# Optimization experiments

Hardware: AMD Instinct MI355X
Metric: run time of the kernel (lower is better)

The kernel has to match this reference:

```python
import jax, jax.numpy as jnp
import numpy as np

B, C, T = 64, 128, 500
N_RES, N_CLASSES = 2048, 10
DECAY_RES, DECAY_CLF = 0.9, 0.9
V_TH_RES, V_TH_CLF = 1.0, 1.0


def setup_inputs() -> dict:
    key = jax.random.key(0)
    k1, k2, k3, k4 = jax.random.split(key, 4)
    x = jax.random.normal(k1, (B, C, T), dtype=jnp.float32)
    # learned / fixed parameters sized per init_kwargs
    W_in = jax.random.normal(k2, (N_RES, C), dtype=jnp.float32) * (1.0 / np.sqrt(C))
    W_res = jax.random.normal(k3, (N_RES, N_RES), dtype=jnp.float32) * (1.0 / np.sqrt(N_RES))
    W_clf = jax.random.normal(k4, (N_CLASSES, N_RES), dtype=jnp.float32) * (1.0 / np.sqrt(N_RES))
    return {"x": x, "W_in": W_in, "W_res": W_res, "W_clf": W_clf}


def reference(x, W_in, W_res, W_clf):
    """x: (B, C, T). Returns (spike_counts (B, n_classes), reservoir_spikes_accum (B, n_reservoir)).
    LIF reservoir + single-voter LIF readout, no STDP updates (use_stdp=False path)."""
    Bb = x.shape[0]
    dtype = x.dtype

    def step(carry, x_t):  # x_t: (B, C)
        v_r, s_prev, v_c = carry
        # reservoir LIF: leak + feedforward input + recurrent spike input
        I = x_t @ W_in.T + s_prev @ W_res.T          # (B, N_RES)
        v_r = DECAY_RES * v_r + I
        s = (v_r >= V_TH_RES).astype(dtype)          # spike
        v_r = v_r * (1.0 - s)                        # reset fired neurons
        # classifier (STDPLayer forward, plasticity disabled)
        v_c = DECAY_CLF * v_c + s @ W_clf.T          # (B, N_CLASSES)
        c = (v_c >= V_TH_CLF).astype(dtype)
        v_c = v_c * (1.0 - c)
        return (v_r, s, v_c), (c, s)

    init = (jnp.zeros((Bb, N_RES), dtype),
            jnp.zeros((Bb, N_RES), dtype),
            jnp.zeros((Bb, N_CLASSES), dtype))
    xs = jnp.moveaxis(x, 2, 0)                       # (T, B, C)
    _, (clf_spikes, res_spikes) = jax.lax.scan(step, init, xs)
    spike_counts = clf_spikes.sum(axis=0)            # (B, N_CLASSES)
    reservoir_spikes_accum = res_spikes.sum(axis=0)  # (B, N_RES)
    return spike_counts, reservoir_spikes_accum
```

## Files before the change

kernel.cpp:

```cpp
#include <hip/hip_runtime.h>
#include <cstdint>
#include <cstddef>

#define B_    64
#define C_    128
#define T_    500
#define NRES  2048
#define NCLS  10

#define NWG   256
#define SL    8
#define NT    1024
#define WROW  520
#define WPIT  (4 * WROW)



#define WS_MASK0   0
#define WS_MASK1   16384
#define WS_CNT1    32768
#define WS_CNT2    34816
#define WS_FLAG    36864
#define WS_WORDS   13312
#define NGRP       8
#define GRPSZ      (NWG / NGRP)
#define NFLAG      16

typedef float v2f __attribute__((ext_vector_type(2)));

struct SMem {
  float    WtT2[SL][WPIT];
  float    WinT2[SL][C_];
  float    xs[B_][C_ + 1];
  unsigned mask[B_][65];
  float    g1buf[SL][B_];
  double   clfred[2][16][NCLS];
};

__global__ void zero_ws_kernel(unsigned* __restrict__ p, int n) {
  int i = blockIdx.x * blockDim.x + threadIdx.x;
  if (i < n) p[i] = 0u;
}

#define ACC2(ACC, WB, M0, M1, JB) do {                                        \
  const unsigned _lo = (unsigned)(((int)((M0) << (31 - (JB)))) >> 31) & (WB); \
  const unsigned _hi = (unsigned)(((int)((M1) << (31 - (JB)))) >> 31) & (WB); \
  v2f _m; _m.x = __uint_as_float(_lo); _m.y = __uint_as_float(_hi);           \
  (ACC) = (ACC) + _m;                                                         \
} while (0)

#define BT_STEP(X, D, MLO) do {                                            \
  const unsigned _y = (unsigned)__shfl_xor((int)(X), (D), 64);             \
  (X) = (b & (D)) ? (((X) & ~(MLO)) | ((_y >> (D)) & (MLO)))               \
                  : (((X) & (MLO)) | ((_y << (D)) & ~(MLO)));              \
} while (0)

#define BT_ALL(X) do {                 \
  BT_STEP(X, 16, 0x0000FFFFu);         \
  BT_STEP(X,  8, 0x00FF00FFu);         \
  BT_STEP(X,  4, 0x0F0F0F0Fu);         \
  BT_STEP(X,  2, 0x33333333u);         \
  BT_STEP(X,  1, 0x55555555u);         \
} while (0)

__global__ void __launch_bounds__(NT, 4)
reservoir_kernel(const float* __restrict__ x, const float* __restrict__ Win,
                 const float* __restrict__ Wres, const float* __restrict__ Wclf,
                 float* __restrict__ out, unsigned char* __restrict__ ws) {
  __shared__ SMem sm;
  const int w   = blockIdx.x;
  const int tid = threadIdx.x;
  const int b   = tid & 63;
  const int wid = tid >> 6;
  const int il  = wid & 7;
  const int h   = wid >> 3;
  const int blk = b & 3;
  const int g   = b >> 2;
  const int bat0 = h * 32 + g * 2;
  const int bat1 = bat0 + 1;
  const int iu  = __builtin_amdgcn_readfirstlane(w * SL + il);

  unsigned* gm0  = (unsigned*)(ws + WS_MASK0);
  unsigned* gm1  = (unsigned*)(ws + WS_MASK1);
  unsigned* cnt1 = (unsigned*)(ws + WS_CNT1 + (w & (NGRP - 1)) * 256);
  unsigned* cnt2 = (unsigned*)(ws + WS_CNT2);
  unsigned* flgb = (unsigned*)(ws + WS_FLAG);
  unsigned* myflag = flgb + (w & (NFLAG - 1)) * 256;

  {
    const int j0 = tid * 16;
    #pragma unroll
    for (int r4 = 0; r4 < 4; ++r4) {
      const int j   = j0 + r4 * 4;
      const int il2 = j >> 11;
      const int pos = j & 2047;
      const int bk  = pos >> 9;
      const int s   = pos & 511;
      const float4 v4 = *(const float4*)(Wres + (size_t)(w * SL + il2) * NRES + pos);
      *(float4*)(&sm.WtT2[il2][bk * WROW + s]) = v4;
    }
  }
  {
    const int il2 = tid >> 7, c = tid & 127;
    sm.WinT2[il2][c] = Win[(size_t)(w * SL + il2) * C_ + c];
  }

  float wcf[NCLS * 2];
  {
    const int j0 = tid * 2;
    #pragma unroll
    for (int c2 = 0; c2 < NCLS; ++c2)
      #pragma unroll
      for (int jj = 0; jj < 2; ++jj)
        wcf[c2 * 2 + jj] = Wclf[(size_t)c2 * NRES + j0 + jj];
  }

  float v = 0.f;
  int   cntr = 0;
  double vc = 0.0;
  int   cntc = 0;

  float xv[8];
  {
    const int p0 = tid * 8;
    #pragma unroll
    for (int r = 0; r < 8; ++r) xv[r] = x[(size_t)(p0 + r) * T_ + 0];
    #pragma unroll
    for (int r = 0; r < 8; ++r) {
      int p = p0 + r;
      sm.xs[p >> 7][p & 127] = xv[r];
    }
  }

  for (int t = 0; t < T_; ++t) {
    unsigned* gprev = (t & 1) ? gm0 : gm1;
    unsigned* gcur  = (t & 1) ? gm1 : gm0;

    {
      const int i32 = b & 31, hh = b >> 5;
      #pragma unroll
      for (int kk = 0; kk < 4; ++kk) {
        const int k = (wid << 2) | kk;
        unsigned xw = __hip_atomic_load(gprev + (k * 32 + i32) * 2 + hh,
                                        __ATOMIC_RELAXED, __HIP_MEMORY_SCOPE_AGENT);
        BT_ALL(xw);
        sm.mask[b][k] = xw;
      }
    }
    __syncthreads();

    if (t + 1 < T_) {
      const int p0 = tid * 8;
      #pragma unroll
      for (int r = 0; r < 8; ++r) xv[r] = x[(size_t)(p0 + r) * T_ + (t + 1)];
    }

    if (h == 0) {
      float g1 = 0.f;
      const float4* __restrict__ winp = (const float4*)&sm.WinT2[il][0];
      #pragma unroll 8
      for (int cq = 0; cq < 32; ++cq) {
        const float4 wv = winp[cq];
        const int c = cq * 4;
        g1 = fmaf(sm.xs[b][c + 0], wv.x, g1);
        g1 = fmaf(sm.xs[b][c + 1], wv.y, g1);
        g1 = fmaf(sm.xs[b][c + 2], wv.z, g1);
        g1 = fmaf(sm.xs[b][c + 3], wv.w, g1);
      }
      sm.g1buf[il][b] = g1;
    }

    v2f acc; acc.x = 0.f; acc.y = 0.f;
    {
      const float*    wbase = &sm.WtT2[il][blk * WROW];
      const unsigned* mr0   = &sm.mask[bat0][blk * 16];
      const unsigned* mr1   = &sm.mask[bat1][blk * 16];
      for (int wq = 0; wq < 16; ++wq) {
        const unsigned m0 = mr0[wq];
        const unsigned m1 = mr1[wq];
        const float4* q = (const float4*)(wbase + wq * 32);
        #pragma unroll
        for (int jq = 0; jq < 8; ++jq) {
          const float4 w4 = q[jq];
          const int jb = jq * 4;
          ACC2(acc, __float_as_uint(w4.x), m0, m1, jb + 0);
          ACC2(acc, __float_as_uint(w4.y), m0, m1, jb + 1);
          ACC2(acc, __float_as_uint(w4.z), m0, m1, jb + 2);
          ACC2(acc, __float_as_uint(w4.w), m0, m1, jb + 3);
        }
      }
    }
    const float aP = acc.x, aQ = acc.y;

    const float p1 = __shfl_xor(aP, 1), q1 = __shfl_xor(aQ, 1);
    const float p2 = __shfl_xor(aP, 2), q2 = __shfl_xor(aQ, 2);
    const float p3 = __shfl_xor(aP, 3), q3 = __shfl_xor(aQ, 3);
    const float g2u0 = __fadd_rn(__fadd_rn(__fadd_rn(aP, p1), p2), p3);
    const float g2u1 = __fadd_rn(__fadd_rn(__fadd_rn(aQ, q1), q2), q3);

    __syncthreads();

    {
      const int src = (b >> 1) * 4;
      const float r0 = __shfl(g2u0, src, 64);
      const float r1 = __shfl(g2u1, src, 64);
      const float g2m = (b & 1) ? r1 : r0;
      const float g1m = sm.g1buf[il][h * 32 + (b & 31)];
      const float I = __fadd_rn(g1m, g2m);
      v = __fadd_rn(__fmul_rn(0.9f, v), I);
      bool s = (b < 32) && (v >= 1.0f);
      if (s) { v = 0.f; cntr++; }
      unsigned long long bal = __ballot(s);
      if (b == 0)
        __hip_atomic_store(gcur + iu * 2 + h, (unsigned)bal,
                           __ATOMIC_RELAXED, __HIP_MEMORY_SCOPE_AGENT);
    }
    __syncthreads();

    if (tid == 0) {
      unsigned old = __hip_atomic_fetch_add(cnt1, 1u, __ATOMIC_RELEASE,
                                            __HIP_MEMORY_SCOPE_AGENT);
      if (old == (unsigned)(t + 1) * GRPSZ - 1u) {
        unsigned old2 = __hip_atomic_fetch_add(cnt2, 1u, __ATOMIC_ACQ_REL,
                                               __HIP_MEMORY_SCOPE_AGENT);
        if (old2 == (unsigned)(t + 1) * NGRP - 1u) {
          #pragma unroll
          for (int f = 0; f < NFLAG; ++f)
            __hip_atomic_store(flgb + f * 256, (unsigned)(t + 1),
                               __ATOMIC_RELEASE, __HIP_MEMORY_SCOPE_AGENT);
        }
      }
    }

    if (w < B_) {
      double pc[NCLS];
      #pragma unroll
      for (int c2 = 0; c2 < NCLS; ++c2) pc[c2] = 0.0;
      if (t > 0) {
        const int j0 = tid * 2;
        unsigned mw = sm.mask[w][j0 >> 5];
        #pragma unroll
        for (int jj = 0; jj < 2; ++jj) {
          if ((mw >> ((j0 + jj) & 31)) & 1u) {
            #pragma unroll
            for (int c2 = 0; c2 < NCLS; ++c2)
              pc[c2] += (double)wcf[c2 * 2 + jj];
          }
        }
      }
      #pragma unroll
      for (int off = 1; off < 64; off <<= 1) {
        #pragma unroll
        for (int c2 = 0; c2 < NCLS; ++c2)
          pc[c2] += __shfl_xor(pc[c2], off, 64);
      }
      if ((tid & 63) == 0) {
        #pragma unroll
        for (int c2 = 0; c2 < NCLS; ++c2) sm.clfred[t & 1][wid][c2] = pc[c2];
      }
    }

    if (w < B_ && tid < NCLS && t >= 2) {
      double sc = 0.0;
      #pragma unroll
      for (int q2 = 0; q2 < 16; ++q2) sc += sm.clfred[(t + 1) & 1][q2][tid];
      vc = 0.9 * vc + sc;
      if (vc >= 1.0) { vc = 0.0; cntc++; }
    }

    if (t + 1 < T_) {
      const int p0 = tid * 8;
      #pragma unroll
      for (int r = 0; r < 8; ++r) {
        int p = p0 + r;
        sm.xs[p >> 7][p & 127] = xv[r];
      }
    }

    if (tid == 0) {
      while (__hip_atomic_load(myflag, __ATOMIC_RELAXED,
                               __HIP_MEMORY_SCOPE_AGENT) < (unsigned)(t + 1))
        __builtin_amdgcn_s_sleep(1);
    }
    __syncthreads();
  }

  if (w < B_ && tid < NCLS) {
    double sc = 0.0;
    #pragma unroll
    for (int q2 = 0; q2 < 16; ++q2) sc += sm.clfred[1][q2][tid];
    vc = 0.9 * vc + sc;
    if (vc >= 1.0) { vc = 0.0; cntc++; }
  }
  {
    const int i32 = b & 31, hh = b >> 5;
    #pragma unroll
    for (int kk = 0; kk < 4; ++kk) {
      const int k = (wid << 2) | kk;
      unsigned xw = __hip_atomic_load(gm1 + (k * 32 + i32) * 2 + hh,
                                      __ATOMIC_RELAXED, __HIP_MEMORY_SCOPE_AGENT);
      BT_ALL(xw);
      sm.mask[b][k] = xw;
    }
  }
  __syncthreads();
  if (w < B_) {
    double pc[NCLS];
    #pragma unroll
    for (int c2 = 0; c2 < NCLS; ++c2) pc[c2] = 0.0;
    const int j0 = tid * 2;
    unsigned mw = sm.mask[w][j0 >> 5];
    #pragma unroll
    for (int jj = 0; jj < 2; ++jj) {
      if ((mw >> ((j0 + jj) & 31)) & 1u) {
        #pragma unroll
        for (int c2 = 0; c2 < NCLS; ++c2)
          pc[c2] += (double)wcf[c2 * 2 + jj];
      }
    }
    #pragma unroll
    for (int off = 1; off < 64; off <<= 1) {
      #pragma unroll
      for (int c2 = 0; c2 < NCLS; ++c2)
        pc[c2] += __shfl_xor(pc[c2], off, 64);
    }
    if ((tid & 63) == 0) {
      #pragma unroll
      for (int c2 = 0; c2 < NCLS; ++c2) sm.clfred[0][wid][c2] = pc[c2];
    }
  }
  __syncthreads();
  if (w < B_ && tid < NCLS) {
    double sc = 0.0;
    #pragma unroll
    for (int q2 = 0; q2 < 16; ++q2) sc += sm.clfred[0][q2][tid];
    vc = 0.9 * vc + sc;
    if (vc >= 1.0) cntc++;
    out[w * NCLS + tid] = (float)cntc;
  }
  if (b < 32)
    out[B_ * NCLS + (size_t)(h * 32 + b) * NRES + w * SL + il] = (float)cntr;
}

extern "C" void kernel_launch(void* const* d_in, const int* in_sizes, int n_in,
                              void* d_out, int out_size, void* d_ws, size_t ws_size,
                              hipStream_t stream) {
  const float* x    = (const float*)d_in[0];
  const float* Win  = (const float*)d_in[1];
  const float* Wres = (const float*)d_in[2];
  const float* Wclf = (const float*)d_in[3];
  float* out = (float*)d_out;
  unsigned char* ws = (unsigned char*)d_ws;

  hipLaunchKernelGGL(zero_ws_kernel, dim3((WS_WORDS + 255) / 256), dim3(256), 0, stream,
                     (unsigned*)ws, WS_WORDS);
  hipLaunchKernelGGL(reservoir_kernel, dim3(NWG), dim3(NT), 0, stream,
                     x, Win, Wres, Wclf, out, ws);
}
```

Baseline: 15.91 ms.

## Replace two-level atomic counter barrier with per-block arrival flags and checker block

Replaces the hierarchical fetch-add grid barrier with per-workgroup arrival slots that a single checker workgroup polls before publishing release flags. It also double-buffers the input slice in shared memory so one in-loop __syncthreads can be removed, computes the input projection in each wave rather than through a shared buffer, and restructures the classifier readout as one wave per class reading Wclf from global memory. The aim is to shorten the per-timestep critical path made of atomics and block barriers. The cost is a single polling workgroup that can become a serialization point, plus repeated global reads of Wclf.

```diff
diff --git a/kernel.cpp b/kernel.cpp
--- a/kernel.cpp
+++ b/kernel.cpp
@@ -18,23 +18,20 @@
 
 #define WS_MASK0   0
 #define WS_MASK1   16384
-#define WS_CNT1    32768
-#define WS_CNT2    34816
-#define WS_FLAG    36864
+#define WS_FLAG    32768
+#define WS_ARR     49152
 #define WS_WORDS   13312
-#define NGRP       8
-#define GRPSZ      (NWG / NGRP)
 #define NFLAG      16
+#define CHKWG      (NWG - 1)
 
 typedef float v2f __attribute__((ext_vector_type(2)));
 
 struct SMem {
   float    WtT2[SL][WPIT];
   float    WinT2[SL][C_];
-  float    xs[B_][C_ + 1];
+  float    xs2[2][B_][C_ + 1];
   unsigned mask[B_][65];
-  float    g1buf[SL][B_];
-  double   clfred[2][16][NCLS];
+  double   clfred2[2][NCLS];
 };
 
 __global__ void zero_ws_kernel(unsigned* __restrict__ p, int n) {
@@ -82,9 +79,8 @@
 
   unsigned* gm0  = (unsigned*)(ws + WS_MASK0);
   unsigned* gm1  = (unsigned*)(ws + WS_MASK1);
-  unsigned* cnt1 = (unsigned*)(ws + WS_CNT1 + (w & (NGRP - 1)) * 256);
-  unsigned* cnt2 = (unsigned*)(ws + WS_CNT2);
   unsigned* flgb = (unsigned*)(ws + WS_FLAG);
+  unsigned* arr  = (unsigned*)(ws + WS_ARR);
   unsigned* myflag = flgb + (w & (NFLAG - 1)) * 256;
 
   {
@@ -105,16 +101,6 @@
     sm.WinT2[il2][c] = Win[(size_t)(w * SL + il2) * C_ + c];
   }
 
-  float wcf[NCLS * 2];
-  {
-    const int j0 = tid * 2;
-    #pragma unroll
-    for (int c2 = 0; c2 < NCLS; ++c2)
-      #pragma unroll
-      for (int jj = 0; jj < 2; ++jj)
-        wcf[c2 * 2 + jj] = Wclf[(size_t)c2 * NRES + j0 + jj];
-  }
-
   float v = 0.f;
   int   cntr = 0;
   double vc = 0.0;
@@ -124,12 +110,13 @@
   {
     const int p0 = tid * 8;
     #pragma unroll
-    for (int r = 0; r < 8; ++r) xv[r] = x[(size_t)(p0 + r) * T_ + 0];
-    #pragma unroll
     for (int r = 0; r < 8; ++r) {
+      float z = x[(size_t)(p0 + r) * T_ + 0];
       int p = p0 + r;
-      sm.xs[p >> 7][p & 127] = xv[r];
-    }
+      sm.xs2[0][p >> 7][p & 127] = z;
+    }
+    #pragma unroll
+    for (int r = 0; r < 8; ++r) xv[r] = x[(size_t)(p0 + r) * T_ + 1];
   }
 
   for (int t = 0; t < T_; ++t) {
@@ -152,22 +139,30 @@
     if (t + 1 < T_) {
       const int p0 = tid * 8;
       #pragma unroll
-      for (int r = 0; r < 8; ++r) xv[r] = x[(size_t)(p0 + r) * T_ + (t + 1)];
-    }
-
-    if (h == 0) {
-      float g1 = 0.f;
+      for (int r = 0; r < 8; ++r) {
+        int p = p0 + r;
+        sm.xs2[(t + 1) & 1][p >> 7][p & 127] = xv[r];
+      }
+      if (t + 2 < T_) {
+        #pragma unroll
+        for (int r = 0; r < 8; ++r) xv[r] = x[(size_t)(p0 + r) * T_ + (t + 2)];
+      }
+    }
+
+    float g1 = 0.f;
+    if (b < 32) {
+      const int bat = h * 32 + b;
       const float4* __restrict__ winp = (const float4*)&sm.WinT2[il][0];
+      const float* __restrict__ xrow = &sm.xs2[t & 1][bat][0];
       #pragma unroll 8
       for (int cq = 0; cq < 32; ++cq) {
         const float4 wv = winp[cq];
         const int c = cq * 4;
-        g1 = fmaf(sm.xs[b][c + 0], wv.x, g1);
-        g1 = fmaf(sm.xs[b][c + 1], wv.y, g1);
-        g1 = fmaf(sm.xs[b][c + 2], wv.z, g1);
-        g1 = fmaf(sm.xs[b][c + 3], wv.w, g1);
-      }
-      sm.g1buf[il][b] = g1;
+        g1 = fmaf(xrow[c + 0], wv.x, g1);
+        g1 = fmaf(xrow[c + 1], wv.y, g1);
+        g1 = fmaf(xrow[c + 2], wv.z, g1);
+        g1 = fmaf(xrow[c + 3], wv.w, g1);
+      }
     }
 
     v2f acc; acc.x = 0.f; acc.y = 0.f;
@@ -198,15 +193,12 @@
     const float g2u0 = __fadd_rn(__fadd_rn(__fadd_rn(aP, p1), p2), p3);
     const float g2u1 = __fadd_rn(__fadd_rn(__fadd_rn(aQ, q1), q2), q3);
 
-    __syncthreads();
-
     {
       const int src = (b >> 1) * 4;
       const float r0 = __shfl(g2u0, src, 64);
       const float r1 = __shfl(g2u1, src, 64);
       const float g2m = (b & 1) ? r1 : r0;
-      const float g1m = sm.g1buf[il][h * 32 + (b & 31)];
-      const float I = __fadd_rn(g1m, g2m);
+      const float I = __fadd_rn(g1, g2m);
       v = __fadd_rn(__fmul_rn(0.9f, v), I);
       bool s = (b < 32) && (v >= 1.0f);
       if (s) { v = 0.f; cntr++; }
@@ -217,64 +209,52 @@
     }
     __syncthreads();
 
-    if (tid == 0) {
-      unsigned old = __hip_atomic_fetch_add(cnt1, 1u, __ATOMIC_RELEASE,
-                                            __HIP_MEMORY_SCOPE_AGENT);
-      if (old == (unsigned)(t + 1) * GRPSZ - 1u) {
-        unsigned old2 = __hip_atomic_fetch_add(cnt2, 1u, __ATOMIC_ACQ_REL,
-                                               __HIP_MEMORY_SCOPE_AGENT);
-        if (old2 == (unsigned)(t + 1) * NGRP - 1u) {
-          #pragma unroll
-          for (int f = 0; f < NFLAG; ++f)
-            __hip_atomic_store(flgb + f * 256, (unsigned)(t + 1),
-                               __ATOMIC_RELEASE, __HIP_MEMORY_SCOPE_AGENT);
+    if (tid == 0)
+      __hip_atomic_store(arr + w * 4, (unsigned)(t + 1),
+                         __ATOMIC_RELEASE, __HIP_MEMORY_SCOPE_AGENT);
+
+    if (w == CHKWG && wid == 0) {
+      const unsigned tgt = (unsigned)(t + 1);
+      for (;;) {
+        unsigned a0 = __hip_atomic_load(arr + (b +   0) * 4, __ATOMIC_RELAXED,
+                                        __HIP_MEMORY_SCOPE_AGENT);
+        unsigned a1 = __hip_atomic_load(arr + (b +  64) * 4, __ATOMIC_RELAXED,
+                                        __HIP_MEMORY_SCOPE_AGENT);
+        unsigned a2 = __hip_atomic_load(arr + (b + 128) * 4, __ATOMIC_RELAXED,
+                                        __HIP_MEMORY_SCOPE_AGENT);
+        unsigned a3 = __hip_atomic_load(arr + (b + 192) * 4, __ATOMIC_RELAXED,
+                                        __HIP_MEMORY_SCOPE_AGENT);
+        bool ok = (a0 >= tgt) & (a1 >= tgt) & (a2 >= tgt) & (a3 >= tgt);
+        if (__all(ok)) break;
+        __builtin_amdgcn_s_sleep(1);
+      }
+      if (b < NFLAG)
+        __hip_atomic_store(flgb + b * 256, (unsigned)(t + 1),
+                           __ATOMIC_RELEASE, __HIP_MEMORY_SCOPE_AGENT);
+    }
+
+    if (w < B_ && wid < NCLS) {
+      double pc = 0.0;
+      if (t > 0) {
+        const float* __restrict__ wc = Wclf + (size_t)wid * NRES + b;
+        #pragma unroll 4
+        for (int q = 0; q < 32; ++q) {
+          const unsigned mw = sm.mask[w][(b >> 5) + 2 * q];
+          const float wv = wc[q * 64];
+          const unsigned keep =
+              (unsigned)(((int)(mw << (31 - (b & 31)))) >> 31);
+          pc += (double)__uint_as_float(keep & __float_as_uint(wv));
         }
       }
-    }
-
-    if (w < B_) {
-      double pc[NCLS];
       #pragma unroll
-      for (int c2 = 0; c2 < NCLS; ++c2) pc[c2] = 0.0;
-      if (t > 0) {
-        const int j0 = tid * 2;
-        unsigned mw = sm.mask[w][j0 >> 5];
-        #pragma unroll
-        for (int jj = 0; jj < 2; ++jj) {
-          if ((mw >> ((j0 + jj) & 31)) & 1u) {
-            #pragma unroll
-            for (int c2 = 0; c2 < NCLS; ++c2)
-              pc[c2] += (double)wcf[c2 * 2 + jj];
-          }
-        }
-      }
-      #pragma unroll
-      for (int off = 1; off < 64; off <<= 1) {
-        #pragma unroll
-        for (int c2 = 0; c2 < NCLS; ++c2)
-          pc[c2] += __shfl_xor(pc[c2], off, 64);
-      }
-      if ((tid & 63) == 0) {
-        #pragma unroll
-        for (int c2 = 0; c2 < NCLS; ++c2) sm.clfred[t & 1][wid][c2] = pc[c2];
-      }
+      for (int off = 1; off < 64; off <<= 1)
+        pc += __shfl_xor(pc, off, 64);
+      if (b == 0) sm.clfred2[t & 1][wid] = pc;
     }
 
     if (w < B_ && tid < NCLS && t >= 2) {
-      double sc = 0.0;
-      #pragma unroll
-      for (int q2 = 0; q2 < 16; ++q2) sc += sm.clfred[(t + 1) & 1][q2][tid];
-      vc = 0.9 * vc + sc;
+      vc = 0.9 * vc + sm.clfred2[(t + 1) & 1][tid];
       if (vc >= 1.0) { vc = 0.0; cntc++; }
-    }
-
-    if (t + 1 < T_) {
-      const int p0 = tid * 8;
-      #pragma unroll
-      for (int r = 0; r < 8; ++r) {
-        int p = p0 + r;
-        sm.xs[p >> 7][p & 127] = xv[r];
-      }
     }
 
     if (tid == 0) {
@@ -286,10 +266,7 @@
   }
 
   if (w < B_ && tid < NCLS) {
-    double sc = 0.0;
-    #pragma unroll
-    for (int q2 = 0; q2 < 16; ++q2) sc += sm.clfred[1][q2][tid];
-    vc = 0.9 * vc + sc;
+    vc = 0.9 * vc + sm.clfred2[1][tid];
     if (vc >= 1.0) { vc = 0.0; cntc++; }
   }
   {
@@ -304,37 +281,27 @@
     }
   }
   __syncthreads();
-  if (w < B_) {
-    double pc[NCLS];
-    #pragma unroll
-    for (int c2 = 0; c2 < NCLS; ++c2) pc[c2] = 0.0;
-    const int j0 = tid * 2;
-    unsigned mw = sm.mask[w][j0 >> 5];
-    #pragma unroll
-    for (int jj = 0; jj < 2; ++jj) {
-      if ((mw >> ((j0 + jj) & 31)) & 1u) {
-        #pragma unroll
-        for (int c2 = 0; c2 < NCLS; ++c2)
-          pc[c2] += (double)wcf[c2 * 2 + jj];
-      }
-    }
-    #pragma unroll
-    for (int off = 1; off < 64; off <<= 1) {
-      #pragma unroll
-      for (int c2 = 0; c2 < NCLS; ++c2)
-        pc[c2] += __shfl_xor(pc[c2], off, 64);
-    }
-    if ((tid & 63) == 0) {
-      #pragma unroll
-      for (int c2 = 0; c2 < NCLS; ++c2) sm.clfred[0][wid][c2] = pc[c2];
-    }
+  if (w < B_ && wid < NCLS) {
+    double pc = 0.0;
+    {
+      const float* __restrict__ wc = Wclf + (size_t)wid * NRES + b;
+      #pragma unroll 4
+      for (int q = 0; q < 32; ++q) {
+        const unsigned mw = sm.mask[w][(b >> 5) + 2 * q];
+        const float wv = wc[q * 64];
+        const unsigned keep =
+            (unsigned)(((int)(mw << (31 - (b & 31)))) >> 31);
+        pc += (double)__uint_as_float(keep & __float_as_uint(wv));
+      }
+    }
+    #pragma unroll
+    for (int off = 1; off < 64; off <<= 1)
+      pc += __shfl_xor(pc, off, 64);
+    if (b == 0) sm.clfred2[0][wid] = pc;
   }
   __syncthreads();
   if (w < B_ && tid < NCLS) {
-    double sc = 0.0;
-    #pragma unroll
-    for (int q2 = 0; q2 < 16; ++q2) sc += sm.clfred[0][q2][tid];
-    vc = 0.9 * vc + sc;
+    vc = 0.9 * vc + sm.clfred2[0][tid];
     if (vc >= 1.0) cntc++;
     out[w * NCLS + tid] = (float)cntc;
   }
```

Measured after the change: 14.03 ms. 1.13x faster.
